# Optimization experiments

Measured on AMD Instinct MI355X. Metric: run time of the kernel, lower is better.

The kernel has to match this reference:

```python
import jax, jax.numpy as jnp
import numpy as np

B, T, C, D = 16, 2048, 1024, 128  # batch, seq, n_embd, head_size

def setup_inputs() -> dict:
    key = jax.random.key(0)
    kx, kq, kk, kv = jax.random.split(key, 4)
    x = jax.random.normal(kx, (B, T, C), dtype=jnp.float32)
    s = 1.0 / np.sqrt(C)
    Wq = jax.random.normal(kq, (C, D), dtype=jnp.float32) * s
    Wk = jax.random.normal(kk, (C, D), dtype=jnp.float32) * s
    Wv = jax.random.normal(kv, (C, D), dtype=jnp.float32) * s
    return {"x": x, "Wq": Wq, "Wk": Wk, "Wv": Wv}

def reference(x, Wq, Wk, Wv):
    # q,k,v: [B,T,D]
    q = jnp.einsum('btc,cd->btd', x, Wq)
    k = jnp.einsum('btc,cd->btd', x, Wk)
    v = jnp.einsum('btc,cd->btd', x, Wv)
    scale = 1.0 / jnp.sqrt(jnp.asarray(q.shape[-1], q.dtype))
    wei = jnp.einsum('bqd,bkd->bqk', q, k) * scale  # [B,T,T]
    causal = jnp.tril(jnp.ones((T, T), dtype=bool))
    wei = jnp.where(causal, wei, -jnp.inf)
    wei = jax.nn.softmax(wei, axis=-1)
    # dropout is identity in eval mode
    out = jnp.einsum('bqk,bkd->bqd', wei, v)  # [B,T,D]
    return out
```

## Files before the change

### kernel.cpp

```cpp
#include <hip/hip_runtime.h>

typedef unsigned short u16;
typedef unsigned int   u32;
typedef __attribute__((ext_vector_type(8)))  __bf16 bf16x8;
typedef __attribute__((ext_vector_type(16))) float  f32x16;
typedef __attribute__((ext_vector_type(4)))  float  fl4;
typedef __attribute__((ext_vector_type(4)))  u16    u16x4;
typedef __attribute__((ext_vector_type(4)))  u32    u32x4;

#define NB 16
#define NT 2048
#define NC 1024
#define ND 128


__device__ __forceinline__ u16 f2bf(float f) {
  u32 u = __builtin_bit_cast(u32, f);
  u = (u + 0x7fffu + ((u >> 16) & 1u)) >> 16;
  return (u16)u;
}

__device__ __forceinline__ u32 pk2(float lo, float hi) {
  return (u32)f2bf(lo) | ((u32)f2bf(hi) << 16);
}

__global__ __launch_bounds__(256) void wprep_k(
    const float* __restrict__ Wq, const float* __restrict__ Wk,
    const float* __restrict__ Wv, u16* __restrict__ wf)
{
  const int cb   = blockIdx.x;
  const int kind = cb >> 2;
  const float* __restrict__ W = (kind == 0) ? Wq : (kind == 1) ? Wk : Wv;
  const int lane = threadIdx.x & 63;
  const int ksq  = threadIdx.x >> 6;
  const int l31 = lane & 31, hi = lane >> 5;
  const int d = (cb & 3) * 32 + l31;
  u16* __restrict__ o = wf + (size_t)cb * 64 * 512;
  #pragma unroll 4
  for (int ii = 0; ii < 16; ++ii) {
    int ks = ksq * 16 + ii;
    int k  = ks * 16 + hi * 8;
    u16x4 p0, p1;
    #pragma unroll
    for (int j = 0; j < 4; ++j) p0[j] = f2bf(W[(size_t)(k + j) * ND + d]);
    #pragma unroll
    for (int j = 0; j < 4; ++j) p1[j] = f2bf(W[(size_t)(k + 4 + j) * ND + d]);
    u16* dst = o + ((size_t)ks * 64 + lane) * 8;
    *(u16x4*)dst = p0;
    *(u16x4*)(dst + 4) = p1;
  }
}

__global__ __launch_bounds__(512, 4) void qkv_fused_k(
    const float* __restrict__ x, const u16* __restrict__ wf,
    u16* __restrict__ qf, u16* __restrict__ kf, u16* __restrict__ vf)
{
  const int blk  = blockIdx.x;
  const int brow = blk >> 1;
  const int h    = blk & 1;
  const int tid  = threadIdx.x;
  const int lane = tid & 63;
  const int wid  = tid >> 6;
  const int rw = wid & 3, cw = wid >> 2;
  const int l31 = lane & 31, hi = lane >> 5;
  const int m0 = brow * 128;
  const int cbg0 = h * 6;

  __shared__ u16 Ab[2][128 * 64];
  __shared__ u16 Bb[2][24 * 512];

  const int arow = tid >> 4;
  const int ac4  = (tid & 15) * 4;
  const float* __restrict__ xr = x + (size_t)(m0 + arow) * NC + ac4;

  fl4 pA0[4], pA1[4];
  bf16x8 pb[3];

  auto issueA = [&](fl4* dst, int bk) {
    #pragma unroll
    for (int p = 0; p < 4; ++p)
      dst[p] = *(const fl4*)(xr + (size_t)p * 32 * NC + bk * 64);
  };
  auto issueB = [&](int bk) {
    #pragma unroll
    for (int i = 0; i < 3; ++i) {
      int idx = i * 512 + tid;
      int cb6 = idx >> 8, ks = (idx >> 6) & 3;
      pb[i] = *(const bf16x8*)(wf + (((size_t)(cbg0 + cb6) * 64 + bk * 4 + ks) * 64 + (idx & 63)) * 8);
    }
  };
  auto writeA = [&](int buf, fl4* src) {
    char* b = (char*)Ab[buf];
    #pragma unroll
    for (int p = 0; p < 4; ++p) {
      int row = p * 32 + arow;
      u16x4 pk;
      pk[0] = f2bf(src[p][0]); pk[1] = f2bf(src[p][1]);
      pk[2] = f2bf(src[p][2]); pk[3] = f2bf(src[p][3]);
      *(u16x4*)(b + row * 128 + ((ac4 * 2) ^ ((row & 7) << 4))) = pk;
    }
  };
  auto writeB = [&](int buf) {
    #pragma unroll
    for (int i = 0; i < 3; ++i)
      *(bf16x8*)&Bb[buf][((size_t)i * 512 + tid) * 8] = pb[i];
  };

  f32x16 acc[3] = {};

  auto compute = [&](int buf) {
    const char* ab = (const char*)Ab[buf];
    #pragma unroll
    for (int ks = 0; ks < 4; ++ks) {
      int row = rw * 32 + l31;
      bf16x8 a = *(const bf16x8*)(ab + row * 128 + ((ks * 32 + hi * 16) ^ ((row & 7) << 4)));
      #pragma unroll
      for (int cb = 0; cb < 3; ++cb) {
        bf16x8 b = *(const bf16x8*)&Bb[buf][((size_t)((cw * 3 + cb) * 4 + ks) * 64 + lane) * 8];
        acc[cb] = __builtin_amdgcn_mfma_f32_32x32x16_bf16(a, b, acc[cb], 0, 0, 0);
      }
    }
  };

  auto ITER = [&](int bk, fl4* sFill, fl4* sNext) {
    if (bk + 2 < 16) issueA(sFill, bk + 2);
    if (bk + 1 < 16) issueB(bk + 1);
    compute(bk & 1);
    if (bk + 1 < 16) { writeA((bk + 1) & 1, sNext); writeB((bk + 1) & 1); }
    __syncthreads();
  };

  issueA(pA0, 0); issueA(pA1, 1); issueB(0);
  writeA(0, pA0); writeB(0);
  __syncthreads();

  #pragma unroll
  for (int i = 0; i < 8; ++i) {
    ITER(2 * i,     pA0, pA1);
    ITER(2 * i + 1, pA1, pA0);
  }

  const int t32 = brow * 4 + rw;
  #pragma unroll
  for (int cb = 0; cb < 3; ++cb) {
    const int colb = h * 192 + cw * 96 + cb * 32;
    const int kind = colb >> 7;
    const int d    = (colb & 127) + l31;
    if (kind < 2) {
      u16* __restrict__ o = kind ? kf : qf;
      const float sc = kind ? 1.0f : 0.12752539240377073f;
      const int ds = d >> 4, b3 = (d >> 3) & 1, j = d & 7;
      u16* __restrict__ base = o + ((size_t)t32 * 8 + ds) * 512 + 32 * b3 * 8 + j;
      #pragma unroll
      for (int r = 0; r < 16; ++r) {
        int crow = (r & 3) + 8 * (r >> 2) + 4 * hi;
        base[crow * 8] = f2bf(acc[cb][r] * sc);
      }
    } else {
      const int dt = (d & 127) >> 5;
      #pragma unroll
      for (int g = 0; g < 4; ++g) {
        int c16   = t32 * 2 + (g >> 1);
        int lanep = l31 + 32 * (g & 1);
        u16x4 pk;
        #pragma unroll
        for (int jj = 0; jj < 4; ++jj) pk[jj] = f2bf(acc[cb][g * 4 + jj]);
        *(u16x4*)(vf + (((size_t)c16 * 4 + dt) * 64 + lanep) * 8 + 4 * hi) = pk;
      }
    }
  }
}

__global__ __launch_bounds__(128, 2) void attn_fwd_k(
    const u16* __restrict__ qw, const u16* __restrict__ kw,
    const u16* __restrict__ vw, float* __restrict__ out)
{
  const int tid  = threadIdx.x;
  const int lane = tid & 63;
  const int w    = tid >> 6;
  const int l31  = lane & 31;
  const int hi   = lane >> 5;

  const int c  = blockIdx.x;
  const int bb = (c >> 6) & 15;
  const int qi = ((c & 63) + ((c >> 8) << 4)) & 63;
  const int q0 = qi * 32;
  const int qrow = q0 + l31;

  const u16* __restrict__ qb = qw + ((size_t)bb * 64 + qi) * 4096;
  const u16* __restrict__ kb = kw + (size_t)bb * 64 * 4096;
  const u16* __restrict__ vb = vw + (size_t)bb * 128 * 2048;

  __shared__ float ofs[64][64];
  __shared__ float mls[2][64];

  bf16x8 qfr[8];
  #pragma unroll
  for (int s = 0; s < 8; ++s)
    qfr[s] = *(const bf16x8*)(qb + ((size_t)s * 64 + lane) * 8);

  f32x16 of[4] = {};
  float m_run = -__builtin_inff();
  float l_run = 0.f;

  const int nsteps = (qi >> 1) + 1;
  for (int s = w; s < nsteps; s += 2) {
    const int kv0 = s * 64;
    const bool masked = (s == nsteps - 1);

    bf16x8 kf0[8], kf1[8];
    #pragma unroll
    for (int t = 0; t < 8; ++t) {
      kf0[t] = *(const bf16x8*)(kb + (((size_t)(2 * s) * 8 + t) * 64 + lane) * 8);
      kf1[t] = *(const bf16x8*)(kb + (((size_t)(2 * s + 1) * 8 + t) * 64 + lane) * 8);
    }
    f32x16 st0 = {}, st1 = {};
    #pragma unroll
    for (int t = 0; t < 8; ++t) {
      st0 = __builtin_amdgcn_mfma_f32_32x32x16_bf16(kf0[t], qfr[t], st0, 0, 0, 0);
      st1 = __builtin_amdgcn_mfma_f32_32x32x16_bf16(kf1[t], qfr[t], st1, 0, 0, 0);
    }
    bf16x8 vfr[4][4];
    #pragma unroll
    for (int ks = 0; ks < 4; ++ks)
      #pragma unroll
      for (int dt = 0; dt < 4; ++dt)
        vfr[dt][ks] = *(const bf16x8*)(vb + (((size_t)((kv0 >> 4) + ks) * 4 + dt) * 64 + lane) * 8);

    if (masked) {
      #pragma unroll
      for (int r = 0; r < 16; ++r) {
        int crow = (r & 3) + 8 * (r >> 2) + 4 * hi;
        st0[r] = (kv0 + crow      <= qrow) ? st0[r] : -1e30f;
        st1[r] = (kv0 + 32 + crow <= qrow) ? st1[r] : -1e30f;
      }
    }

    float pmax = -1e30f;
    #pragma unroll
    for (int r = 0; r < 16; ++r) pmax = fmaxf(pmax, fmaxf(st0[r], st1[r]));
    pmax = fmaxf(pmax, __shfl_xor(pmax, 32, 64));

    const bool no_rescale = (pmax <= m_run);
    const float m_new = fmaxf(m_run, pmax);
    const float fac = __builtin_amdgcn_exp2f(m_run - m_new);
    float rsum = 0.f;
    #pragma unroll
    for (int r = 0; r < 16; ++r) {
      st0[r] = __builtin_amdgcn_exp2f(st0[r] - m_new);
      st1[r] = __builtin_amdgcn_exp2f(st1[r] - m_new);
      rsum += st0[r] + st1[r];
    }
    rsum += __shfl_xor(rsum, 32, 64);
    l_run = l_run * fac + rsum;
    m_run = m_new;

    if (!__all(no_rescale)) {
      #pragma unroll
      for (int r = 0; r < 16; ++r) {
        float fr = __shfl(fac, (r & 3) + 8 * (r >> 2) + 4 * hi, 64);
        #pragma unroll
        for (int dt = 0; dt < 4; ++dt) of[dt][r] *= fr;
      }
    }

    u32x4 pa[4];
    #pragma unroll
    for (int g = 0; g < 4; ++g) {
      const float* sp = (g < 2) ? (const float*)&st0 : (const float*)&st1;
      const int o8 = (g & 1) * 8;
      u32 a0 = pk2(sp[o8 + 0], sp[o8 + 1]);
      u32 a1 = pk2(sp[o8 + 2], sp[o8 + 3]);
      u32 b0 = pk2(sp[o8 + 4], sp[o8 + 5]);
      u32 b1 = pk2(sp[o8 + 6], sp[o8 + 7]);
      u32 ta0 = __shfl_xor(a0, 32, 64);
      u32 ta1 = __shfl_xor(a1, 32, 64);
      u32 tb0 = __shfl_xor(b0, 32, 64);
      u32 tb1 = __shfl_xor(b1, 32, 64);
      pa[g][0] = hi ? tb0 : a0;
      pa[g][1] = hi ? tb1 : a1;
      pa[g][2] = hi ? b0  : ta0;
      pa[g][3] = hi ? b1  : ta1;
    }

    #pragma unroll
    for (int ks = 0; ks < 4; ++ks) {
      bf16x8 paf = __builtin_bit_cast(bf16x8, pa[ks]);
      #pragma unroll
      for (int dt = 0; dt < 4; ++dt)
        of[dt] = __builtin_amdgcn_mfma_f32_32x32x16_bf16(paf, vfr[dt][ks], of[dt], 0, 0, 0);
    }
  }

  if (w == 1) {
    #pragma unroll
    for (int dt = 0; dt < 4; ++dt)
      #pragma unroll
      for (int r = 0; r < 16; ++r)
        ofs[dt * 16 + r][lane] = of[dt][r];
    mls[0][lane] = m_run;
    mls[1][lane] = l_run;
  }
  __syncthreads();
  if (w == 0) {
    const float m1 = mls[0][l31];
    const float l1 = mls[1][l31];
    const float mt = fmaxf(m_run, m1);
    const float f0 = __builtin_amdgcn_exp2f(m_run - mt);
    const float f1 = __builtin_amdgcn_exp2f(m1 - mt);
    const float lt = l_run * f0 + l1 * f1;
    const float rl = 1.0f / lt;
    #pragma unroll
    for (int r = 0; r < 16; ++r) {
      int crow = (r & 3) + 8 * (r >> 2) + 4 * hi;
      float f0r = __shfl(f0, crow, 64);
      float f1r = __shfl(f1, crow, 64);
      float lr  = __shfl(rl, crow, 64);
      #pragma unroll
      for (int dt = 0; dt < 4; ++dt)
        out[((size_t)(bb * NT + q0 + crow)) * ND + dt * 32 + l31] =
            (of[dt][r] * f0r + ofs[dt * 16 + r][lane] * f1r) * lr;
    }
  }
}

extern "C" void kernel_launch(void* const* d_in, const int* in_sizes, int n_in,
                              void* d_out, int out_size, void* d_ws, size_t ws_size,
                              hipStream_t stream) {
  (void)in_sizes; (void)n_in; (void)out_size; (void)ws_size;
  const float* x  = (const float*)d_in[0];
  const float* Wq = (const float*)d_in[1];
  const float* Wk = (const float*)d_in[2];
  const float* Wv = (const float*)d_in[3];
  float* out = (float*)d_out;

  u16* qws = (u16*)d_ws;
  u16* kws = qws + (size_t)NB * NT * ND;
  u16* vws = kws + (size_t)NB * NT * ND;
  u16* wfs = vws + (size_t)NB * NT * ND;

  wprep_k<<<dim3(12), dim3(256), 0, stream>>>(Wq, Wk, Wv, wfs);
  qkv_fused_k<<<dim3(512), dim3(512), 0, stream>>>(x, wfs, qws, kws, vws);
  attn_fwd_k<<<dim3(1024), dim3(128), 0, stream>>>(qws, kws, vws, out);
}
```

Before: 102.5 us.

## Restructure QKV projection into per-kind blocks with direct global B-fragment loads

The fused QKV projection kernel is replaced. It used 512 blocks of 512 threads, each covering 128 rows by 192 columns with double-buffered LDS for both x and the weights. The new kernel uses 768 blocks of 256 threads, one per 128-row tile per Q/K/V kind. Each wave computes a 64x64 tile with weight fragments read straight from global memory into registers, and only x is staged in a single-buffered LDS tile. Each x tile is now read three times instead of twice. The change also drops the double buffering, adds two barriers per k-step, and switches the conversion to the native bf16 cast.

```diff
diff --git a/kernel.cpp b/kernel.cpp
--- a/kernel.cpp
+++ b/kernel.cpp
@@ -51,121 +51,105 @@
   }
 }
 
-__global__ __launch_bounds__(512, 4) void qkv_fused_k(
+__global__ __launch_bounds__(256, 3) void qkv_proj_k(
     const float* __restrict__ x, const u16* __restrict__ wf,
     u16* __restrict__ qf, u16* __restrict__ kf, u16* __restrict__ vf)
 {
-  const int blk  = blockIdx.x;
-  const int brow = blk >> 1;
-  const int h    = blk & 1;
+  const int L    = blockIdx.x;
+  const int rt   = L & 255;
+  const int kind = L >> 8;
   const int tid  = threadIdx.x;
   const int lane = tid & 63;
   const int wid  = tid >> 6;
-  const int rw = wid & 3, cw = wid >> 2;
+  const int wr = wid >> 1, wc = wid & 1;
   const int l31 = lane & 31, hi = lane >> 5;
-  const int m0 = brow * 128;
-  const int cbg0 = h * 6;
-
-  __shared__ u16 Ab[2][128 * 64];
-  __shared__ u16 Bb[2][24 * 512];
-
-  const int arow = tid >> 4;
-  const int ac4  = (tid & 15) * 4;
-  const float* __restrict__ xr = x + (size_t)(m0 + arow) * NC + ac4;
-
-  fl4 pA0[4], pA1[4];
-  bf16x8 pb[3];
-
-  auto issueA = [&](fl4* dst, int bk) {
-    #pragma unroll
-    for (int p = 0; p < 4; ++p)
-      dst[p] = *(const fl4*)(xr + (size_t)p * 32 * NC + bk * 64);
+  const int m0 = rt * 128;
+
+  __shared__ u16 As[128 * 64];
+
+  const int srow = tid >> 4;
+  const int sc4  = (tid & 15) * 4;
+  const float* __restrict__ xr = x + (size_t)(m0 + srow) * NC + sc4;
+
+  fl4 pA[8];
+  auto issueA = [&](int k0) {
+    #pragma unroll
+    for (int it = 0; it < 8; ++it)
+      pA[it] = *(const fl4*)(xr + (size_t)it * 16 * NC + k0);
   };
-  auto issueB = [&](int bk) {
-    #pragma unroll
-    for (int i = 0; i < 3; ++i) {
-      int idx = i * 512 + tid;
-      int cb6 = idx >> 8, ks = (idx >> 6) & 3;
-      pb[i] = *(const bf16x8*)(wf + (((size_t)(cbg0 + cb6) * 64 + bk * 4 + ks) * 64 + (idx & 63)) * 8);
+  auto writeA = [&]() {
+    char* b = (char*)As;
+    #pragma unroll
+    for (int it = 0; it < 8; ++it) {
+      int row = it * 16 + srow;
+      u16x4 pk;
+      pk[0] = __builtin_bit_cast(u16, (__bf16)pA[it][0]);
+      pk[1] = __builtin_bit_cast(u16, (__bf16)pA[it][1]);
+      pk[2] = __builtin_bit_cast(u16, (__bf16)pA[it][2]);
+      pk[3] = __builtin_bit_cast(u16, (__bf16)pA[it][3]);
+      *(u16x4*)(b + row * 128 + ((sc4 * 2) ^ ((row & 7) << 4))) = pk;
     }
   };
-  auto writeA = [&](int buf, fl4* src) {
-    char* b = (char*)Ab[buf];
-    #pragma unroll
-    for (int p = 0; p < 4; ++p) {
-      int row = p * 32 + arow;
-      u16x4 pk;
-      pk[0] = f2bf(src[p][0]); pk[1] = f2bf(src[p][1]);
-      pk[2] = f2bf(src[p][2]); pk[3] = f2bf(src[p][3]);
-      *(u16x4*)(b + row * 128 + ((ac4 * 2) ^ ((row & 7) << 4))) = pk;
-    }
-  };
-  auto writeB = [&](int buf) {
-    #pragma unroll
-    for (int i = 0; i < 3; ++i)
-      *(bf16x8*)&Bb[buf][((size_t)i * 512 + tid) * 8] = pb[i];
-  };
-
-  f32x16 acc[3] = {};
-
-  auto compute = [&](int buf) {
-    const char* ab = (const char*)Ab[buf];
+
+  const u16* __restrict__ wfb = wf + ((size_t)(kind * 4 + wc * 2) * 64) * 512 + lane * 8;
+
+  f32x16 acc[2][2] = {};
+
+  issueA(0);
+  for (int k = 0; k < 16; ++k) {
+    writeA();
+    if (k < 15) issueA((k + 1) * 64);
+    __syncthreads();
+
+    bf16x8 bfr[2][4];
+    #pragma unroll
+    for (int cb = 0; cb < 2; ++cb)
+      #pragma unroll
+      for (int ks = 0; ks < 4; ++ks)
+        bfr[cb][ks] = *(const bf16x8*)(wfb + ((size_t)cb * 64 + k * 4 + ks) * 512);
+
+    const char* ab = (const char*)As;
     #pragma unroll
     for (int ks = 0; ks < 4; ++ks) {
-      int row = rw * 32 + l31;
-      bf16x8 a = *(const bf16x8*)(ab + row * 128 + ((ks * 32 + hi * 16) ^ ((row & 7) << 4)));
-      #pragma unroll
-      for (int cb = 0; cb < 3; ++cb) {
-        bf16x8 b = *(const bf16x8*)&Bb[buf][((size_t)((cw * 3 + cb) * 4 + ks) * 64 + lane) * 8];
-        acc[cb] = __builtin_amdgcn_mfma_f32_32x32x16_bf16(a, b, acc[cb], 0, 0, 0);
+      #pragma unroll
+      for (int fm = 0; fm < 2; ++fm) {
+        int row = wr * 64 + fm * 32 + l31;
+        bf16x8 a = *(const bf16x8*)(ab + row * 128 + ((ks * 32 + hi * 16) ^ ((row & 7) << 4)));
+        #pragma unroll
+        for (int cb = 0; cb < 2; ++cb)
+          acc[fm][cb] = __builtin_amdgcn_mfma_f32_32x32x16_bf16(a, bfr[cb][ks], acc[fm][cb], 0, 0, 0);
       }
     }
-  };
-
-  auto ITER = [&](int bk, fl4* sFill, fl4* sNext) {
-    if (bk + 2 < 16) issueA(sFill, bk + 2);
-    if (bk + 1 < 16) issueB(bk + 1);
-    compute(bk & 1);
-    if (bk + 1 < 16) { writeA((bk + 1) & 1, sNext); writeB((bk + 1) & 1); }
     __syncthreads();
-  };
-
-  issueA(pA0, 0); issueA(pA1, 1); issueB(0);
-  writeA(0, pA0); writeB(0);
-  __syncthreads();
+  }
 
   #pragma unroll
-  for (int i = 0; i < 8; ++i) {
-    ITER(2 * i,     pA0, pA1);
-    ITER(2 * i + 1, pA1, pA0);
-  }
-
-  const int t32 = brow * 4 + rw;
-  #pragma unroll
-  for (int cb = 0; cb < 3; ++cb) {
-    const int colb = h * 192 + cw * 96 + cb * 32;
-    const int kind = colb >> 7;
-    const int d    = (colb & 127) + l31;
-    if (kind < 2) {
-      u16* __restrict__ o = kind ? kf : qf;
-      const float sc = kind ? 1.0f : 0.12752539240377073f;
-      const int ds = d >> 4, b3 = (d >> 3) & 1, j = d & 7;
-      u16* __restrict__ base = o + ((size_t)t32 * 8 + ds) * 512 + 32 * b3 * 8 + j;
-      #pragma unroll
-      for (int r = 0; r < 16; ++r) {
-        int crow = (r & 3) + 8 * (r >> 2) + 4 * hi;
-        base[crow * 8] = f2bf(acc[cb][r] * sc);
-      }
-    } else {
-      const int dt = (d & 127) >> 5;
-      #pragma unroll
-      for (int g = 0; g < 4; ++g) {
-        int c16   = t32 * 2 + (g >> 1);
-        int lanep = l31 + 32 * (g & 1);
-        u16x4 pk;
+  for (int fm = 0; fm < 2; ++fm) {
+    const int t32 = rt * 4 + wr * 2 + fm;
+    #pragma unroll
+    for (int cb = 0; cb < 2; ++cb) {
+      const int d = wc * 64 + cb * 32 + l31;
+      if (kind < 2) {
+        u16* __restrict__ o = kind ? kf : qf;
+        const float sc = kind ? 1.0f : 0.12752539240377073f;
+        const int ds = d >> 4, b3 = (d >> 3) & 1, j = d & 7;
+        u16* __restrict__ base = o + ((size_t)t32 * 8 + ds) * 512 + 32 * b3 * 8 + j;
         #pragma unroll
-        for (int jj = 0; jj < 4; ++jj) pk[jj] = f2bf(acc[cb][g * 4 + jj]);
-        *(u16x4*)(vf + (((size_t)c16 * 4 + dt) * 64 + lanep) * 8 + 4 * hi) = pk;
+        for (int r = 0; r < 16; ++r) {
+          int crow = (r & 3) + 8 * (r >> 2) + 4 * hi;
+          base[crow * 8] = f2bf(acc[fm][cb][r] * sc);
+        }
+      } else {
+        const int dt = d >> 5;
+        #pragma unroll
+        for (int g = 0; g < 4; ++g) {
+          int c16   = t32 * 2 + (g >> 1);
+          int lanep = l31 + 32 * (g & 1);
+          u16x4 pk;
+          #pragma unroll
+          for (int jj = 0; jj < 4; ++jj) pk[jj] = f2bf(acc[fm][cb][g * 4 + jj]);
+          *(u16x4*)(vf + (((size_t)c16 * 4 + dt) * 64 + lanep) * 8 + 4 * hi) = pk;
+        }
       }
     }
   }
@@ -340,6 +324,6 @@
   u16* wfs = vws + (size_t)NB * NT * ND;
 
   wprep_k<<<dim3(12), dim3(256), 0, stream>>>(Wq, Wk, Wv, wfs);
-  qkv_fused_k<<<dim3(512), dim3(512), 0, stream>>>(x, wfs, qws, kws, vws);
+  qkv_proj_k<<<dim3(768), dim3(256), 0, stream>>>(x, wfs, qws, kws, vws);
   attn_fwd_k<<<dim3(1024), dim3(128), 0, stream>>>(qws, kws, vws, out);
 }
```

Result: slower. 109.2 us (+6.5%).
